# Performance work log

Hardware: AMD Instinct MI355X
Metric: run time of the kernel (lower is better)

The kernel has to match this reference:

```python
import jax, jax.numpy as jnp
import numpy as np

B_SZ, L, D_MODEL = 2, 1024, 1024
D_INNER, D_STATE, D_CONV = 2048, 16, 4
EPS = 1e-6


def setup_inputs() -> dict:
    key = jax.random.key(0)
    ks = jax.random.split(key, 8)
    def n(k, shape, scale=0.02):
        return jax.random.normal(k, shape, jnp.float32) * scale
    return {
        "x": jax.random.normal(ks[0], (B_SZ, L, D_MODEL), jnp.float32),
        "W_in": n(ks[1], (D_MODEL, 2 * D_INNER)),
        "b_in": jnp.zeros((2 * D_INNER,), jnp.float32),
        "conv_w": n(ks[2], (D_INNER, 1, D_CONV), 0.2),
        "conv_b": jnp.zeros((D_INNER,), jnp.float32),
        "W_xp": n(ks[3], (D_INNER, 2 * D_STATE)),
        "b_xp": jnp.zeros((2 * D_STATE,), jnp.float32),
        "W_dt": n(ks[4], (D_INNER, D_INNER)),
        "b_dt": jnp.full((D_INNER,), -1.0, jnp.float32),
        # torch code does log(randn) (NaN-prone); use log of positive uniform instead
        "A_log": jnp.log(jax.random.uniform(ks[5], (D_INNER, D_STATE), jnp.float32, 0.5, 1.5)),
        "D_skip": jnp.ones((D_INNER,), jnp.float32),
        "W_out": n(ks[6], (D_INNER, D_MODEL)),
        "b_out": jnp.zeros((D_MODEL,), jnp.float32),
        "alpha": jnp.ones((D_MODEL,), jnp.float32),
        "beta": jnp.zeros((D_MODEL,), jnp.float32),
    }


def _selective_scan(xc, delta, A, Bm, Cm, D_skip):
    # xc, delta: (B,L,di); A: (di,ds); Bm, Cm: (B,L,ds)
    dA = jnp.exp(delta[..., None] * A)                     # (B,L,di,ds)
    dBx = (delta * xc)[..., None] * Bm[:, :, None, :]      # (B,L,di,ds)
    h0 = jnp.zeros((xc.shape[0], xc.shape[2], A.shape[1]), xc.dtype)

    def step(h, inp):
        dA_t, dBx_t, C_t = inp
        h = dA_t * h + dBx_t                               # (B,di,ds)
        y_t = jnp.einsum('bds,bs->bd', h, C_t)
        return h, y_t

    _, ys = jax.lax.scan(
        step, h0,
        (dA.transpose(1, 0, 2, 3), dBx.transpose(1, 0, 2, 3), Cm.transpose(1, 0, 2)))
    y = ys.transpose(1, 0, 2)                              # (B,L,di)
    return y + D_skip * xc


def _layernorm(r, alpha, beta):
    # torch LayerNormalization: unbiased std, eps added to std
    mean = jnp.mean(r, axis=-1, keepdims=True)
    diff = r - mean
    var_unb = jnp.sum(diff * diff, axis=-1, keepdims=True) / (r.shape[-1] - 1)
    std = jnp.sqrt(var_unb)
    return alpha * diff / (std + EPS) + beta


def reference(x, W_in, b_in, conv_w, conv_b, W_xp, b_xp, W_dt, b_dt,
              A_log, D_skip, W_out, b_out, alpha, beta):
    residual = x
    xz = x @ W_in + b_in                                   # (B,L,2*di)
    x_in, z = jnp.split(xz, 2, axis=-1)

    # depthwise causal conv1d (torch pads d_conv-1 both sides, slices [:L])
    xt = x_in.transpose(0, 2, 1)                           # (B,di,L)
    xt = jax.lax.conv_general_dilated(
        xt, conv_w, window_strides=(1,), padding=[(D_CONV - 1, 0)],
        feature_group_count=D_INNER, dimension_numbers=('NCH', 'OIH', 'NCH'))
    xt = xt + conv_b[None, :, None]
    x_conv = jax.nn.silu(xt.transpose(0, 2, 1))            # (B,L,di)

    x_proj_out = x_conv @ W_xp + b_xp                      # (B,L,2*ds)
    Bm, Cm = jnp.split(x_proj_out, 2, axis=-1)
    delta = jax.nn.softplus(x_conv @ W_dt + b_dt)          # (B,L,di)
    A = -jnp.exp(A_log)

    y = _selective_scan(x_conv, delta, A, Bm, Cm, D_skip)
    y = y * jax.nn.silu(z)
    out = y @ W_out + b_out                                # (B,L,D)
    return _layernorm(residual + out, alpha, beta)
```

## Files before the change

kernel.cpp:

```cpp
#include <hip/hip_runtime.h>
#include <math.h>

#define B_SZ    2
#define L_SEQ   1024
#define DMODEL  1024
#define DINNER  2048
#define DSTATE  16
#define EPSV    1e-6f

#define CCH 64
#define CS  (L_SEQ / CCH)
#define DT  16
#define SSTR 1040

typedef short  bf16x8  __attribute__((ext_vector_type(8)));
typedef float  floatx4 __attribute__((ext_vector_type(4)));
typedef unsigned short ushort8v __attribute__((ext_vector_type(8)));

extern "C" __device__ float __ocml_native_exp2_f32(float);
extern "C" __device__ float __ocml_native_log2_f32(float);

__device__ __forceinline__ float nexp2(float x) { return __ocml_native_exp2_f32(x); }

__device__ __forceinline__ float softplus_f(float v) {
    if (v > 20.f) return v;
    return 0.69314718f * __ocml_native_log2_f32(1.f + nexp2(v * 1.44269504f));
}
__device__ __forceinline__ float silu_f(float z) {
    return z / (1.f + nexp2(z * -1.44269504f));
}

__device__ __forceinline__ unsigned short f2bf(float f) {
    unsigned int u = __float_as_uint(f);
    unsigned int r = (u + 0x7FFFu + ((u >> 16) & 1u)) >> 16;
    return (unsigned short)r;
}
__device__ __forceinline__ float bf2f(unsigned short u) {
    return __uint_as_float(((unsigned int)u) << 16);
}

__device__ __forceinline__ void gload_lds16(const unsigned short* g, unsigned short* l) {
    __builtin_amdgcn_global_load_lds(
        (const __attribute__((address_space(1))) unsigned int*)g,
        (__attribute__((address_space(3))) unsigned int*)l,
        16, 0, 0);
}

__global__ __launch_bounds__(256) void prep_kernel(
    const float* __restrict__ x, unsigned short* __restrict__ x_bf,
    const float* __restrict__ W_in, unsigned short* __restrict__ W_in_t,
    const float* __restrict__ W_dt, unsigned short* __restrict__ W_dt_t,
    const float* __restrict__ W_out, unsigned short* __restrict__ W_out_t)
{
    const int bid = blockIdx.x;
    if (bid >= 10240) {
        const int i = (bid - 10240) * 256 + threadIdx.x;
        float4 v = ((const float4*)x)[i];
        ushort4 o = { f2bf(v.x), f2bf(v.y), f2bf(v.z), f2bf(v.w) };
        ((ushort4*)x_bf)[i] = o;
        return;
    }
    __shared__ float tile[32][33];
    const float* W; unsigned short* Wt; int K, N, t;
    if (bid < 4096)      { W = W_in;  Wt = W_in_t;  K = 1024; N = 4096; t = bid; }
    else if (bid < 8192) { W = W_dt;  Wt = W_dt_t;  K = 2048; N = 2048; t = bid - 4096; }
    else                 { W = W_out; Wt = W_out_t; K = 2048; N = 1024; t = bid - 8192; }
    const int nx = N >> 5;
    const int n0 = (t % nx) * 32;
    const int k0 = (t / nx) * 32;
    const int c = threadIdx.x & 31;
    const int r = threadIdx.x >> 5;
#pragma unroll
    for (int i = 0; i < 4; ++i)
        tile[r + 8 * i][c] = W[(size_t)(k0 + r + 8 * i) * N + n0 + c];
    __syncthreads();
#pragma unroll
    for (int i = 0; i < 4; ++i)
        Wt[(size_t)(n0 + r + 8 * i) * K + k0 + c] = f2bf(tile[c][r + 8 * i]);
}

__global__ __launch_bounds__(256) void transp_bf16(
    const unsigned short* __restrict__ in, unsigned short* __restrict__ outp)
{
    __shared__ unsigned short tile[64][66];
    const int bx = blockIdx.x & 31;
    const int by = blockIdx.x >> 5;
    const int m0 = bx * 64, d0 = by * 64;
    const int tid = threadIdx.x;
    const int r = tid >> 3;
    const int c = (tid & 7) * 8;
#pragma unroll
    for (int i = 0; i < 2; ++i) {
        const int row = r + i * 32;
        ushort8v v = *(const ushort8v*)&in[(size_t)(m0 + row) * DINNER + d0 + c];
        *(ushort8v*)&tile[row][c] = v;
    }
    __syncthreads();
#pragma unroll
    for (int i = 0; i < 2; ++i) {
        const int dd = r + i * 32;
        ushort8v o;
#pragma unroll
        for (int k = 0; k < 8; ++k) o[k] = tile[c + k][dd];
        *(ushort8v*)&outp[(size_t)(d0 + dd) * (B_SZ * L_SEQ) + m0 + c] = o;
    }
}

template <int TM, int TN, int MODE, int MINW>
__global__ __launch_bounds__(256, MINW) void gemm_bf16(
    const unsigned short* __restrict__ A, const unsigned short* __restrict__ Bt,
    const float* __restrict__ bias, const float* __restrict__ resid,
    float* __restrict__ C, unsigned short* __restrict__ zout,
    int M, int N, int K)
{
    constexpr int MI = TM / 32;
    constexpr int NJ = TN / 32;
    constexpr int NINSTR = (TM + TN) / 8;
    constexpr int NI = NINSTR / 4;

    __shared__ unsigned short As[TM * 64];
    __shared__ unsigned short Bs[TN * 64];

    const int tid  = threadIdx.x;
    const int wave = tid >> 6;
    const int lane = tid & 63;
    const int m0 = blockIdx.y * TM;
    const int n0 = blockIdx.x * TN;
    const int wm = (wave >> 1) * (TM / 2);
    const int wn = (wave & 1) * (TN / 2);
    const int fr = lane & 15;
    const int kg = lane >> 4;

    const unsigned short* gq[NI];
    unsigned short* lq[NI];
#pragma unroll
    for (int q = 0; q < NI; ++q) {
        const int idx = wave * NI + q;
        const int r0i = idx * 8;
        const int sub = lane >> 3;
        const int pos = lane & 7;
        if (r0i < TM) {
            const int row = r0i + sub;
            const int ch  = pos ^ (row & 7);
            gq[q] = A + (size_t)(m0 + row) * K + ch * 8;
            lq[q] = &As[r0i * 64];
        } else {
            const int rb = r0i - TM + sub;
            const int ch = pos ^ (rb & 7);
            gq[q] = Bt + (size_t)(n0 + rb) * K + ch * 8;
            lq[q] = &Bs[(r0i - TM) * 64];
        }
    }

    floatx4 acc[MI][NJ] = {};

#pragma unroll
    for (int q = 0; q < NI; ++q) gload_lds16(gq[q], lq[q]);

    for (int kt = 0; kt < K; kt += 64) {
        __syncthreads();

#pragma unroll
        for (int ks = 0; ks < 2; ++ks) {
            const int cq = (ks << 2) | kg;
            bf16x8 af[MI], bfv[NJ];
#pragma unroll
            for (int i = 0; i < MI; ++i) {
                const int row = wm + i * 16 + fr;
                af[i] = *(const bf16x8*)&As[row * 64 + ((cq ^ (row & 7)) << 3)];
            }
#pragma unroll
            for (int j = 0; j < NJ; ++j) {
                const int row = wn + j * 16 + fr;
                bfv[j] = *(const bf16x8*)&Bs[row * 64 + ((cq ^ (row & 7)) << 3)];
            }
#pragma unroll
            for (int i = 0; i < MI; ++i)
#pragma unroll
                for (int j = 0; j < NJ; ++j)
                    acc[i][j] = __builtin_amdgcn_mfma_f32_16x16x32_bf16(
                        af[i], bfv[j], acc[i][j], 0, 0, 0);
        }

        if (kt + 64 < K) {
            __syncthreads();
#pragma unroll
            for (int q = 0; q < NI; ++q) gload_lds16(gq[q] + kt + 64, lq[q]);
        }
    }

    const int rq = (lane >> 4) * 4;
    if (MODE == 4) {
        unsigned short* Ct = (unsigned short*)C;
#pragma unroll
        for (int i = 0; i < MI; ++i) {
#pragma unroll
            for (int j = 0; j < NJ; ++j) {
                const int col = n0 + wn + j * 16 + fr;
                const float bv = bias[col];
                const int row0 = m0 + wm + i * 16 + rq;
                ushort4 o;
#pragma unroll
                for (int r = 0; r < 4; ++r)
                    (&o.x)[r] = f2bf(softplus_f(acc[i][j][r] + bv));
                *(ushort4*)&Ct[(size_t)col * M + row0] = o;
            }
        }
    } else if (MODE == 5) {
        if (n0 < DINNER) {
#pragma unroll
            for (int i = 0; i < MI; ++i) {
#pragma unroll
                for (int j = 0; j < NJ; ++j) {
                    const int col = n0 + wn + j * 16 + fr;
                    const float bv = bias[col];
#pragma unroll
                    for (int r = 0; r < 4; ++r) {
                        const int row = m0 + wm + i * 16 + rq + r;
                        C[(size_t)row * DINNER + col] = acc[i][j][r] + bv;
                    }
                }
            }
        } else {
#pragma unroll
            for (int i = 0; i < MI; ++i) {
#pragma unroll
                for (int j = 0; j < NJ; ++j) {
                    const int col = n0 + wn + j * 16 + fr;
                    const float bv = bias[col];
                    const int row0 = m0 + wm + i * 16 + rq;
                    ushort4 o;
#pragma unroll
                    for (int r = 0; r < 4; ++r)
                        (&o.x)[r] = f2bf(silu_f(acc[i][j][r] + bv));
                    *(ushort4*)&zout[(size_t)(col - DINNER) * M + row0] = o;
                }
            }
        }
    } else {
#pragma unroll
        for (int i = 0; i < MI; ++i) {
#pragma unroll
            for (int j = 0; j < NJ; ++j) {
                const int col = n0 + wn + j * 16 + fr;
                const float bv = bias[col];
#pragma unroll
                for (int r = 0; r < 4; ++r) {
                    const int row = m0 + wm + i * 16 + rq + r;
                    float v = acc[i][j][r] + bv;
                    if (MODE == 1) {
                        v = softplus_f(v);
                    } else if (MODE == 2) {
                        v += resid[(size_t)row * N + col];
                    }
                    C[(size_t)row * N + col] = v;
                }
            }
        }
    }
}

#define CROWS 4
__global__ __launch_bounds__(256) void conv_xproj(
    const float* __restrict__ x_in, const float* __restrict__ conv_w,
    const float* __restrict__ conv_b, const float* __restrict__ W_xp,
    const float* __restrict__ b_xp,
    unsigned short* __restrict__ x_conv_bf, float* __restrict__ BC)
{
    __shared__ float sxc[CROWS][DINNER];
    __shared__ float red[8][CROWS][32];

    const int tid = threadIdx.x;
    const int r0 = blockIdx.x * CROWS;
    const int c8 = tid * 8;

    float wt[8][4];
#pragma unroll
    for (int ci = 0; ci < 8; ++ci) {
        float4 w4 = *(const float4*)&conv_w[(c8 + ci) * 4];
        wt[ci][0] = w4.x; wt[ci][1] = w4.y; wt[ci][2] = w4.z; wt[ci][3] = w4.w;
    }
    float cb[8];
    *(float4*)&cb[0] = *(const float4*)&conv_b[c8];
    *(float4*)&cb[4] = *(const float4*)&conv_b[c8 + 4];

#pragma unroll
    for (int rr = 0; rr < CROWS; ++rr) {
        const int row = r0 + rr;
        const int l = row & (L_SEQ - 1);
        float acc[8];
#pragma unroll
        for (int ci = 0; ci < 8; ++ci) acc[ci] = cb[ci];
#pragma unroll
        for (int h = 0; h < 4; ++h) {
            const int lsrc = l - 3 + h;
            if (lsrc >= 0) {
                float4 a = *(const float4*)&x_in[(size_t)(row - 3 + h) * DINNER + c8];
                float4 b = *(const float4*)&x_in[(size_t)(row - 3 + h) * DINNER + c8 + 4];
                acc[0] += a.x * wt[0][h]; acc[1] += a.y * wt[1][h];
                acc[2] += a.z * wt[2][h]; acc[3] += a.w * wt[3][h];
                acc[4] += b.x * wt[4][h]; acc[5] += b.y * wt[5][h];
                acc[6] += b.z * wt[6][h]; acc[7] += b.w * wt[7][h];
            }
        }
        float o[8];
        ushort8v ob;
#pragma unroll
        for (int ci = 0; ci < 8; ++ci) {
            o[ci] = silu_f(acc[ci]);
            sxc[rr][c8 + ci] = o[ci];
            ob[ci] = (short)f2bf(o[ci]);
        }
        *(ushort8v*)&x_conv_bf[(size_t)row * DINNER + c8] = ob;
    }
    __syncthreads();

    const int n = tid & 31;
    const int g = tid >> 5;
    float p[CROWS] = {};
    const int k0 = g * 256;
#pragma unroll 4
    for (int k = k0; k < k0 + 256; ++k) {
        const float wv = W_xp[k * 32 + n];
        p[0] += sxc[0][k] * wv;
        p[1] += sxc[1][k] * wv;
        p[2] += sxc[2][k] * wv;
        p[3] += sxc[3][k] * wv;
    }
#pragma unroll
    for (int rr = 0; rr < CROWS; ++rr) red[g][rr][n] = p[rr];
    __syncthreads();
    if (tid < CROWS * 32) {
        const int rr = tid >> 5;
        const int n2 = tid & 31;
        float s = b_xp[n2];
#pragma unroll
        for (int gg = 0; gg < 8; ++gg) s += red[gg][rr][n2];
        BC[(size_t)(r0 + rr) * 32 + n2] = s;
    }
}

__global__ __launch_bounds__(1024, 4) void scan_kernel(
    const unsigned short* __restrict__ deltaT,
    const unsigned short* __restrict__ xcT,
    const float* __restrict__ BC, const float* __restrict__ A_log,
    const float* __restrict__ D_skip, const unsigned short* __restrict__ zt,
    unsigned short* __restrict__ y_bf)
{
    __shared__ unsigned short sH[DSTATE * SSTR];
    __shared__ float sDsum[CCH * DT];

    const int tid = threadIdx.x;
    const int dl  = tid & (DT - 1);
    const int c   = tid >> 4;
    const int b   = blockIdx.x >> 7;
    const int d0  = (blockIdx.x & 127) * DT;
    const int d   = d0 + dl;

    const int l0 = c * CS;
    const int row0 = b * L_SEQ + l0;

    const unsigned short* dpt = deltaT + (size_t)d * (B_SZ * L_SEQ) + row0;
    bf16x8 dv0 = *(const bf16x8*)dpt;
    bf16x8 dv1 = *(const bf16x8*)(dpt + 8);
    const unsigned short* xpt = xcT + (size_t)d * (B_SZ * L_SEQ) + row0;
    bf16x8 xv0 = *(const bf16x8*)xpt;
    bf16x8 xv1 = *(const bf16x8*)(xpt + 8);
    const unsigned short* gpt = zt + (size_t)d * (B_SZ * L_SEQ) + row0;
    bf16x8 gv0 = *(const bf16x8*)gpt;
    bf16x8 gv1 = *(const bf16x8*)(gpt + 8);

    float Al[DSTATE];
#pragma unroll
    for (int s = 0; s < DSTATE; ++s)
        Al[s] = -__expf(A_log[d * DSTATE + s]) * 1.44269504f;
    const float Dsk = D_skip[d];

    float dts[CS], xcs[CS];
    float dsum = 0.f;
#pragma unroll
    for (int k = 0; k < 8; ++k) {
        dts[k]     = bf2f((unsigned short)dv0[k]);
        dts[8 + k] = bf2f((unsigned short)dv1[k]);
        xcs[k]     = bf2f((unsigned short)xv0[k]);
        xcs[8 + k] = bf2f((unsigned short)xv1[k]);
    }
#pragma unroll
    for (int k = 0; k < CS; ++k) dsum += dts[k];

    float h[DSTATE];
#pragma unroll
    for (int s = 0; s < DSTATE; ++s) h[s] = 0.f;

    const float* bcp = BC + (size_t)row0 * 32;

#pragma unroll 4
    for (int j = 0; j < CS; ++j) {
        const float dt = dts[j];
        const float xc = xcs[j];
        float Bv[DSTATE];
        *(float4*)&Bv[0]  = *(const float4*)(bcp + j * 32 + 0);
        *(float4*)&Bv[4]  = *(const float4*)(bcp + j * 32 + 4);
        *(float4*)&Bv[8]  = *(const float4*)(bcp + j * 32 + 8);
        *(float4*)&Bv[12] = *(const float4*)(bcp + j * 32 + 12);
        const float dlx = dt * xc;
#pragma unroll
        for (int s = 0; s < DSTATE; ++s) {
            const float e = nexp2(dt * Al[s]);
            h[s] = e * h[s] + dlx * Bv[s];
        }
    }
#pragma unroll
    for (int s = 0; s < DSTATE; ++s)
        sH[s * SSTR + tid] = f2bf(h[s]);
    sDsum[tid] = dsum;
    __syncthreads();

    if (tid < DSTATE * DT) {
        const int dl2 = tid & (DT - 1);
        const int s2  = tid >> 4;
        const float Alc = -__expf(A_log[(d0 + dl2) * DSTATE + s2]) * 1.44269504f;
        float hh = 0.f;
        for (int c2 = 0; c2 < CCH; ++c2) {
            const int idx = s2 * SSTR + c2 * DT + dl2;
            const float a  = nexp2(Alc * sDsum[c2 * DT + dl2]);
            const float he = bf2f(sH[idx]);
            sH[idx] = f2bf(hh);
            hh = a * hh + he;
        }
    }
    __syncthreads();

#pragma unroll
    for (int s = 0; s < DSTATE; ++s) h[s] = bf2f(sH[s * SSTR + tid]);

    unsigned short* yp = y_bf + (size_t)row0 * DINNER + d;
#pragma unroll
    for (int j = 0; j < 8; ++j) {
        const float dt = dts[j];
        const float xc = xcs[j];
        const float g  = bf2f((unsigned short)gv0[j]);
        float Bv[DSTATE], Cv[DSTATE];
        *(float4*)&Bv[0]  = *(const float4*)(bcp + j * 32 + 0);
        *(float4*)&Bv[4]  = *(const float4*)(bcp + j * 32 + 4);
        *(float4*)&Bv[8]  = *(const float4*)(bcp + j * 32 + 8);
        *(float4*)&Bv[12] = *(const float4*)(bcp + j * 32 + 12);
        *(float4*)&Cv[0]  = *(const float4*)(bcp + j * 32 + 16);
        *(float4*)&Cv[4]  = *(const float4*)(bcp + j * 32 + 20);
        *(float4*)&Cv[8]  = *(const float4*)(bcp + j * 32 + 24);
        *(float4*)&Cv[12] = *(const float4*)(bcp + j * 32 + 28);
        const float dlx = dt * xc;
        float y = Dsk * xc;
#pragma unroll
        for (int s = 0; s < DSTATE; ++s) {
            const float e = nexp2(dt * Al[s]);
            h[s] = e * h[s] + dlx * Bv[s];
            y += h[s] * Cv[s];
        }
        yp[j * DINNER] = f2bf(y * g);
    }
#pragma unroll
    for (int j2 = 0; j2 < 8; ++j2) {
        const int j = j2 + 8;
        const float dt = dts[j];
        const float xc = xcs[j];
        const float g  = bf2f((unsigned short)gv1[j2]);
        float Bv[DSTATE], Cv[DSTATE];
        *(float4*)&Bv[0]  = *(const float4*)(bcp + j * 32 + 0);
        *(float4*)&Bv[4]  = *(const float4*)(bcp + j * 32 + 4);
        *(float4*)&Bv[8]  = *(const float4*)(bcp + j * 32 + 8);
        *(float4*)&Bv[12] = *(const float4*)(bcp + j * 32 + 12);
        *(float4*)&Cv[0]  = *(const float4*)(bcp + j * 32 + 16);
        *(float4*)&Cv[4]  = *(const float4*)(bcp + j * 32 + 20);
        *(float4*)&Cv[8]  = *(const float4*)(bcp + j * 32 + 24);
        *(float4*)&Cv[12] = *(const float4*)(bcp + j * 32 + 28);
        const float dlx = dt * xc;
        float y = Dsk * xc;
#pragma unroll
        for (int s = 0; s < DSTATE; ++s) {
            const float e = nexp2(dt * Al[s]);
            h[s] = e * h[s] + dlx * Bv[s];
            y += h[s] * Cv[s];
        }
        yp[j * DINNER] = f2bf(y * g);
    }
}

__global__ __launch_bounds__(256) void layernorm_kernel(
    const float* __restrict__ t, const float* __restrict__ alpha,
    const float* __restrict__ beta, float* __restrict__ out)
{
    __shared__ float sred[4];
    __shared__ float sred2[4];
    const int row = blockIdx.x;
    const int tid = threadIdx.x;
    const float* r = t + (size_t)row * DMODEL;

    float4 v = *(const float4*)&r[tid * 4];
    float lsum = v.x + v.y + v.z + v.w;
#pragma unroll
    for (int m = 1; m < 64; m <<= 1) lsum += __shfl_xor(lsum, m);
    if ((tid & 63) == 0) sred[tid >> 6] = lsum;
    __syncthreads();
    const float mean = (sred[0] + sred[1] + sred[2] + sred[3]) * (1.f / DMODEL);

    const float dx = v.x - mean, dy = v.y - mean, dz = v.z - mean, dw = v.w - mean;
    float ls2 = dx * dx + dy * dy + dz * dz + dw * dw;
#pragma unroll
    for (int m = 1; m < 64; m <<= 1) ls2 += __shfl_xor(ls2, m);
    if ((tid & 63) == 0) sred2[tid >> 6] = ls2;
    __syncthreads();
    const float var = (sred2[0] + sred2[1] + sred2[2] + sred2[3]) * (1.f / (DMODEL - 1));
    const float inv = 1.f / (sqrtf(var) + EPSV);

    float4 a4 = *(const float4*)&alpha[tid * 4];
    float4 b4 = *(const float4*)&beta[tid * 4];
    float4 o;
    o.x = a4.x * dx * inv + b4.x;
    o.y = a4.y * dy * inv + b4.y;
    o.z = a4.z * dz * inv + b4.z;
    o.w = a4.w * dw * inv + b4.w;
    *(float4*)&out[(size_t)row * DMODEL + tid * 4] = o;
}

extern "C" void kernel_launch(void* const* d_in, const int* in_sizes, int n_in,
                              void* d_out, int out_size, void* d_ws, size_t ws_size,
                              hipStream_t stream)
{
    const float* x      = (const float*)d_in[0];
    const float* W_in   = (const float*)d_in[1];
    const float* b_in   = (const float*)d_in[2];
    const float* conv_w = (const float*)d_in[3];
    const float* conv_b = (const float*)d_in[4];
    const float* W_xp   = (const float*)d_in[5];
    const float* b_xp   = (const float*)d_in[6];
    const float* W_dt   = (const float*)d_in[7];
    const float* b_dt   = (const float*)d_in[8];
    const float* A_log  = (const float*)d_in[9];
    const float* D_skip = (const float*)d_in[10];
    const float* W_out  = (const float*)d_in[11];
    const float* b_out  = (const float*)d_in[12];
    const float* alpha  = (const float*)d_in[13];
    const float* beta   = (const float*)d_in[14];
    float* out = (float*)d_out;

    const size_t M = (size_t)B_SZ * L_SEQ;
    char* ws = (char*)d_ws;
    float* x_in    = (float*)(ws + 0);
    unsigned short* zt = (unsigned short*)(ws + (16u << 20));
    unsigned short* deltaT = (unsigned short*)(ws + (48u << 20));
    float* BC      = (float*)(ws + (64u << 20));
    unsigned short* x_bf       = (unsigned short*)(ws + (64u << 20) + (512u << 10));
    unsigned short* W_in_t     = (unsigned short*)(ws + (69u << 20));
    unsigned short* W_dt_t     = (unsigned short*)(ws + (77u << 20));
    unsigned short* W_out_t    = (unsigned short*)(ws + (85u << 20));
    unsigned short* x_conv_bf  = (unsigned short*)(ws + (89u << 20));
    unsigned short* xcT        = (unsigned short*)(ws + (24u << 20));
    unsigned short* ygate_bf   = (unsigned short*)(ws + (77u << 20));
    float* tpre = x_in;

    const dim3 blk(256);

    prep_kernel<<<dim3(12288), blk, 0, stream>>>(
        x, x_bf, W_in, W_in_t, W_dt, W_dt_t, W_out, W_out_t);

    gemm_bf16<128, 128, 5, 2><<<dim3(4096 / 128, 2048 / 128), blk, 0, stream>>>(
        x_bf, W_in_t, b_in, nullptr, x_in, zt, 2048, 4096, 1024);

    conv_xproj<<<dim3((unsigned)(M / CROWS)), blk, 0, stream>>>(
        x_in, conv_w, conv_b, W_xp, b_xp, x_conv_bf, BC);

    transp_bf16<<<dim3(1024), blk, 0, stream>>>(x_conv_bf, xcT);

    gemm_bf16<128, 64, 4, 3><<<dim3(2048 / 64, 2048 / 128), blk, 0, stream>>>(
        x_conv_bf, W_dt_t, b_dt, nullptr, (float*)deltaT, nullptr, 2048, 2048, 2048);

    scan_kernel<<<dim3(B_SZ * (DINNER / DT)), dim3(1024), 0, stream>>>(
        deltaT, xcT, BC, A_log, D_skip, zt, ygate_bf);

    gemm_bf16<64, 64, 2, 3><<<dim3(1024 / 64, 2048 / 64), blk, 0, stream>>>(
        ygate_bf, W_out_t, b_out, x, tpre, nullptr, 2048, 1024, 2048);

    layernorm_kernel<<<dim3((unsigned)M), blk, 0, stream>>>(tpre, alpha, beta, out);
}
```

Measured before the change: 269.6 us.

## Fuse x bf16 conversion into in-proj GEMM and transpose into delta GEMM launch

The in-projection GEMM now reads fp32 x directly, converting it to bf16 while staging the A tile into LDS. This removes the separate x→bf16 pass from the prep kernel. The standalone x_conv transpose kernel is folded into the delta GEMM launch as extra blocks on a 1D grid, which removes one launch. In exchange, A loads in the in-proj GEMM become synchronous register round-trips instead of direct global-to-LDS loads, so more fp32 traffic passes through registers on each K step.

```diff
diff --git a/kernel.cpp b/kernel.cpp
--- a/kernel.cpp
+++ b/kernel.cpp
@@ -47,19 +47,11 @@
 }
 
 __global__ __launch_bounds__(256) void prep_kernel(
-    const float* __restrict__ x, unsigned short* __restrict__ x_bf,
     const float* __restrict__ W_in, unsigned short* __restrict__ W_in_t,
     const float* __restrict__ W_dt, unsigned short* __restrict__ W_dt_t,
     const float* __restrict__ W_out, unsigned short* __restrict__ W_out_t)
 {
     const int bid = blockIdx.x;
-    if (bid >= 10240) {
-        const int i = (bid - 10240) * 256 + threadIdx.x;
-        float4 v = ((const float4*)x)[i];
-        ushort4 o = { f2bf(v.x), f2bf(v.y), f2bf(v.z), f2bf(v.w) };
-        ((ushort4*)x_bf)[i] = o;
-        return;
-    }
     __shared__ float tile[32][33];
     const float* W; unsigned short* Wt; int K, N, t;
     if (bid < 4096)      { W = W_in;  Wt = W_in_t;  K = 1024; N = 4096; t = bid; }
@@ -79,53 +71,54 @@
         Wt[(size_t)(n0 + r + 8 * i) * K + k0 + c] = f2bf(tile[c][r + 8 * i]);
 }
 
-__global__ __launch_bounds__(256) void transp_bf16(
-    const unsigned short* __restrict__ in, unsigned short* __restrict__ outp)
-{
-    __shared__ unsigned short tile[64][66];
-    const int bx = blockIdx.x & 31;
-    const int by = blockIdx.x >> 5;
-    const int m0 = bx * 64, d0 = by * 64;
-    const int tid = threadIdx.x;
-    const int r = tid >> 3;
-    const int c = (tid & 7) * 8;
-#pragma unroll
-    for (int i = 0; i < 2; ++i) {
-        const int row = r + i * 32;
-        ushort8v v = *(const ushort8v*)&in[(size_t)(m0 + row) * DINNER + d0 + c];
-        *(ushort8v*)&tile[row][c] = v;
-    }
-    __syncthreads();
-#pragma unroll
-    for (int i = 0; i < 2; ++i) {
-        const int dd = r + i * 32;
-        ushort8v o;
-#pragma unroll
-        for (int k = 0; k < 8; ++k) o[k] = tile[c + k][dd];
-        *(ushort8v*)&outp[(size_t)(d0 + dd) * (B_SZ * L_SEQ) + m0 + c] = o;
-    }
-}
-
-template <int TM, int TN, int MODE, int MINW>
+template <int TM, int TN, int MODE, int MINW, bool AF32, int NGEMM>
 __global__ __launch_bounds__(256, MINW) void gemm_bf16(
-    const unsigned short* __restrict__ A, const unsigned short* __restrict__ Bt,
+    const void* __restrict__ Araw, const unsigned short* __restrict__ Bt,
     const float* __restrict__ bias, const float* __restrict__ resid,
     float* __restrict__ C, unsigned short* __restrict__ zout,
+    const unsigned short* __restrict__ tin, unsigned short* __restrict__ tout,
     int M, int N, int K)
 {
     constexpr int MI = TM / 32;
     constexpr int NJ = TN / 32;
-    constexpr int NINSTR = (TM + TN) / 8;
-    constexpr int NI = NINSTR / 4;
+    constexpr int NI  = (AF32 ? TN : TM + TN) / 32;
+    constexpr int ASL = AF32 ? TM / 32 : 0;
 
     __shared__ unsigned short As[TM * 64];
     __shared__ unsigned short Bs[TN * 64];
 
     const int tid  = threadIdx.x;
+
+    if (NGEMM != 0 && (int)blockIdx.x >= NGEMM) {
+        unsigned short (*tile)[66] = (unsigned short (*)[66])As;
+        const int t = blockIdx.x - NGEMM;
+        const int m0t = (t & 31) * 64;
+        const int d0t = (t >> 5) * 64;
+        const int r = tid >> 3;
+        const int c = (tid & 7) * 8;
+#pragma unroll
+        for (int i = 0; i < 2; ++i) {
+            const int row = r + i * 32;
+            ushort8v v = *(const ushort8v*)&tin[(size_t)(m0t + row) * DINNER + d0t + c];
+            *(ushort8v*)&tile[row][c] = v;
+        }
+        __syncthreads();
+#pragma unroll
+        for (int i = 0; i < 2; ++i) {
+            const int dd = r + i * 32;
+            ushort8v o;
+#pragma unroll
+            for (int k = 0; k < 8; ++k) o[k] = tile[c + k][dd];
+            *(ushort8v*)&tout[(size_t)(d0t + dd) * (B_SZ * L_SEQ) + m0t + c] = o;
+        }
+        return;
+    }
+
     const int wave = tid >> 6;
     const int lane = tid & 63;
-    const int m0 = blockIdx.y * TM;
-    const int n0 = blockIdx.x * TN;
+    const int nx = N / TN;
+    const int m0 = (NGEMM != 0 ? (int)blockIdx.x / nx : (int)blockIdx.y) * TM;
+    const int n0 = (NGEMM != 0 ? (int)blockIdx.x % nx : (int)blockIdx.x) * TN;
     const int wm = (wave >> 1) * (TM / 2);
     const int wn = (wave & 1) * (TN / 2);
     const int fr = lane & 15;
@@ -135,27 +128,56 @@
     unsigned short* lq[NI];
 #pragma unroll
     for (int q = 0; q < NI; ++q) {
-        const int idx = wave * NI + q;
-        const int r0i = idx * 8;
+        const int r0i = (wave * NI + q) * 8;
         const int sub = lane >> 3;
         const int pos = lane & 7;
-        if (r0i < TM) {
-            const int row = r0i + sub;
+        const int rA  = AF32 ? (TM + r0i) : r0i;
+        if (rA < TM) {
+            const int row = rA + sub;
             const int ch  = pos ^ (row & 7);
-            gq[q] = A + (size_t)(m0 + row) * K + ch * 8;
-            lq[q] = &As[r0i * 64];
+            gq[q] = (const unsigned short*)Araw + (size_t)(m0 + row) * K + ch * 8;
+            lq[q] = &As[rA * 64];
         } else {
-            const int rb = r0i - TM + sub;
+            const int rb = rA - TM + sub;
             const int ch = pos ^ (rb & 7);
             gq[q] = Bt + (size_t)(n0 + rb) * K + ch * 8;
-            lq[q] = &Bs[(r0i - TM) * 64];
-        }
-    }
+            lq[q] = &Bs[(rA - TM) * 64];
+        }
+    }
+
+    int offsA[ASL ? ASL : 1];
+    unsigned short* lpA[ASL ? ASL : 1];
+    if (AF32) {
+#pragma unroll
+        for (int i = 0; i < ASL; ++i) {
+            const int slot = i * 256 + tid;
+            const int row  = slot >> 3;
+            const int ch   = slot & 7;
+            const int pos  = ch ^ (row & 7);
+            offsA[i] = (m0 + row) * K + ch * 8;
+            lpA[i]   = &As[row * 64 + pos * 8];
+        }
+    }
+
+    auto stage = [&](int kt) {
+#pragma unroll
+        for (int q = 0; q < NI; ++q) gload_lds16(gq[q] + kt, lq[q]);
+        if (AF32) {
+            const float* Af = (const float*)Araw;
+#pragma unroll
+            for (int i = 0; i < ASL; ++i) {
+                float4 a0 = *(const float4*)(Af + offsA[i] + kt);
+                float4 a1 = *(const float4*)(Af + offsA[i] + kt + 4);
+                ushort8v o = { f2bf(a0.x), f2bf(a0.y), f2bf(a0.z), f2bf(a0.w),
+                               f2bf(a1.x), f2bf(a1.y), f2bf(a1.z), f2bf(a1.w) };
+                *(ushort8v*)lpA[i] = o;
+            }
+        }
+    };
 
     floatx4 acc[MI][NJ] = {};
 
-#pragma unroll
-    for (int q = 0; q < NI; ++q) gload_lds16(gq[q], lq[q]);
+    stage(0);
 
     for (int kt = 0; kt < K; kt += 64) {
         __syncthreads();
@@ -184,8 +206,7 @@
 
         if (kt + 64 < K) {
             __syncthreads();
-#pragma unroll
-            for (int q = 0; q < NI; ++q) gload_lds16(gq[q] + kt + 64, lq[q]);
+            stage(kt + 64);
         }
     }
 
@@ -550,7 +571,6 @@
     unsigned short* zt = (unsigned short*)(ws + (16u << 20));
     unsigned short* deltaT = (unsigned short*)(ws + (48u << 20));
     float* BC      = (float*)(ws + (64u << 20));
-    unsigned short* x_bf       = (unsigned short*)(ws + (64u << 20) + (512u << 10));
     unsigned short* W_in_t     = (unsigned short*)(ws + (69u << 20));
     unsigned short* W_dt_t     = (unsigned short*)(ws + (77u << 20));
     unsigned short* W_out_t    = (unsigned short*)(ws + (85u << 20));
@@ -561,25 +581,26 @@
 
     const dim3 blk(256);
 
-    prep_kernel<<<dim3(12288), blk, 0, stream>>>(
-        x, x_bf, W_in, W_in_t, W_dt, W_dt_t, W_out, W_out_t);
-
-    gemm_bf16<128, 128, 5, 2><<<dim3(4096 / 128, 2048 / 128), blk, 0, stream>>>(
-        x_bf, W_in_t, b_in, nullptr, x_in, zt, 2048, 4096, 1024);
+    prep_kernel<<<dim3(10240), blk, 0, stream>>>(
+        W_in, W_in_t, W_dt, W_dt_t, W_out, W_out_t);
+
+    gemm_bf16<128, 128, 5, 2, true, 0><<<dim3(4096 / 128, 2048 / 128), blk, 0, stream>>>(
+        (const void*)x, W_in_t, b_in, nullptr, x_in, zt, nullptr, nullptr,
+        2048, 4096, 1024);
 
     conv_xproj<<<dim3((unsigned)(M / CROWS)), blk, 0, stream>>>(
         x_in, conv_w, conv_b, W_xp, b_xp, x_conv_bf, BC);
 
-    transp_bf16<<<dim3(1024), blk, 0, stream>>>(x_conv_bf, xcT);
-
-    gemm_bf16<128, 64, 4, 3><<<dim3(2048 / 64, 2048 / 128), blk, 0, stream>>>(
-        x_conv_bf, W_dt_t, b_dt, nullptr, (float*)deltaT, nullptr, 2048, 2048, 2048);
+    gemm_bf16<128, 64, 4, 3, false, 512><<<dim3(512 + 1024), blk, 0, stream>>>(
+        x_conv_bf, W_dt_t, b_dt, nullptr, (float*)deltaT, nullptr,
+        x_conv_bf, xcT, 2048, 2048, 2048);
 
     scan_kernel<<<dim3(B_SZ * (DINNER / DT)), dim3(1024), 0, stream>>>(
         deltaT, xcT, BC, A_log, D_skip, zt, ygate_bf);
 
-    gemm_bf16<64, 64, 2, 3><<<dim3(1024 / 64, 2048 / 64), blk, 0, stream>>>(
-        ygate_bf, W_out_t, b_out, x, tpre, nullptr, 2048, 1024, 2048);
+    gemm_bf16<64, 64, 2, 3, false, 0><<<dim3(1024 / 64, 2048 / 64), blk, 0, stream>>>(
+        ygate_bf, W_out_t, b_out, x, tpre, nullptr, nullptr, nullptr,
+        2048, 1024, 2048);
 
     layernorm_kernel<<<dim3((unsigned)M), blk, 0, stream>>>(tpre, alpha, beta, out);
 }
```

Measured after the change: 288.2 us. +6.9%, slower.
